# Kernel tuning notes

Measured on AMD Instinct MI355X. Metric: run time of the kernel, lower is better.

## Reference

```python
import jax, jax.numpy as jnp
import numpy as np

HEAD = 16
DIM = 1024
HEAD_DIM = DIM // HEAD


def setup_inputs() -> dict:
    key = jax.random.key(0)
    k1, k2, k3, k4 = jax.random.split(key, 4)
    x = jax.random.normal(k1, (2, 2048, DIM), dtype=jnp.float32)
    # nn.Linear(dim, 3*dim, bias=False): weight [3*dim, dim]
    w_qkv = jax.random.normal(k2, (3 * DIM, DIM), dtype=jnp.float32) * (DIM ** -0.5)
    # output proj nn.Linear(dim, dim)
    w_out = jax.random.normal(k3, (DIM, DIM), dtype=jnp.float32) * (DIM ** -0.5)
    b_out = jax.random.normal(k4, (DIM,), dtype=jnp.float32) * 0.01
    return {"x": x, "w_qkv": w_qkv, "w_out": w_out, "b_out": b_out}


def reference(x, w_qkv, w_out, b_out):
    b, s, _ = x.shape
    scale = HEAD_DIM ** -0.5
    qkv = jnp.einsum('bsd,ed->bse', x, w_qkv)  # [b, s, 3*dim]
    q, k, v = jnp.split(qkv, 3, axis=-1)
    def split_heads(t):
        return t.reshape(b, s, HEAD, HEAD_DIM).transpose(0, 2, 1, 3)  # b h s d
    q, k, v = split_heads(q), split_heads(k), split_heads(v)
    scores = jnp.einsum('bhqd,bhkd->bhqk', q, k) * scale
    attn = jax.nn.softmax(scores, axis=-1)
    out = jnp.einsum('bhqk,bhkd->bhqd', attn, v)
    out = out.transpose(0, 2, 1, 3).reshape(b, s, DIM)
    out = jnp.einsum('bsd,ed->bse', out, w_out) + b_out
    return out
```

## Files before the change

kernel.cpp:

```cpp
#include <hip/hip_runtime.h>
#include <hip/hip_bf16.h>
#include <stdint.h>

typedef __bf16 bf16_t;
typedef __attribute__((ext_vector_type(8))) __bf16 bf16x8;
typedef __attribute__((ext_vector_type(4))) __bf16 bf16x4v;
typedef __attribute__((ext_vector_type(4))) float f32x4;

#define GLOBAL_AS __attribute__((address_space(1)))
#define LDS_AS __attribute__((address_space(3)))

__device__ __forceinline__ void gload_lds16(const bf16_t* g, bf16_t* l) {
  __builtin_amdgcn_global_load_lds((const GLOBAL_AS void*)g, (LDS_AS void*)l, 16, 0, 0);
}

__device__ __forceinline__ uint32_t pk2(float a, float b) {
  union { bf16_t h[2]; uint32_t u; } x;
  x.h[0] = (bf16_t)a; x.h[1] = (bf16_t)b;
  return x.u;
}

__device__ __forceinline__ bf16x8 xpose8(bf16x8 v, int l) {
  union { bf16x8 v; uint32_t u[4]; } tv; tv.v = v;
  uint32_t a0 = __shfl_xor((int)tv.u[2], 4, 64);
  uint32_t a1 = __shfl_xor((int)tv.u[3], 4, 64);
  uint32_t a2 = __shfl_xor((int)tv.u[0], 4, 64);
  uint32_t a3 = __shfl_xor((int)tv.u[1], 4, 64);
  bool s4 = (l & 4) != 0;
  uint32_t n0 = s4 ? a0 : tv.u[0];
  uint32_t n1 = s4 ? a1 : tv.u[1];
  uint32_t n2 = s4 ? tv.u[2] : a2;
  uint32_t n3 = s4 ? tv.u[3] : a3;
  uint32_t b0 = __shfl_xor((int)n1, 2, 64);
  uint32_t b1 = __shfl_xor((int)n0, 2, 64);
  uint32_t b2 = __shfl_xor((int)n3, 2, 64);
  uint32_t b3 = __shfl_xor((int)n2, 2, 64);
  bool s2 = (l & 2) != 0;
  uint32_t m0 = s2 ? b0 : n0;
  uint32_t m1 = s2 ? n1 : b1;
  uint32_t m2 = s2 ? b2 : n2;
  uint32_t m3 = s2 ? n3 : b3;
  uint32_t c0 = __shfl_xor((int)m0, 1, 64);
  uint32_t c1 = __shfl_xor((int)m1, 1, 64);
  uint32_t c2 = __shfl_xor((int)m2, 1, 64);
  uint32_t c3 = __shfl_xor((int)m3, 1, 64);
  bool odd = (l & 1) != 0;
  union { uint32_t u[4]; bf16x8 v; } tw;
  tw.u[0] = odd ? ((m0 & 0xFFFF0000u) | (c0 >> 16)) : ((m0 & 0xFFFFu) | (c0 << 16));
  tw.u[1] = odd ? ((m1 & 0xFFFF0000u) | (c1 >> 16)) : ((m1 & 0xFFFFu) | (c1 << 16));
  tw.u[2] = odd ? ((m2 & 0xFFFF0000u) | (c2 >> 16)) : ((m2 & 0xFFFFu) | (c2 << 16));
  tw.u[3] = odd ? ((m3 & 0xFFFF0000u) | (c3 >> 16)) : ((m3 & 0xFFFFu) | (c3 << 16));
  return tw.v;
}

__global__ void cvt_f32_bf16(const float* __restrict__ in, bf16_t* __restrict__ out, int n) {
  int i = (blockIdx.x * 256 + threadIdx.x) * 4;
  if (i + 3 < n) {
    float4 v = *(const float4*)(in + i);
    bf16x4v o;
    o[0] = (bf16_t)v.x; o[1] = (bf16_t)v.y; o[2] = (bf16_t)v.z; o[3] = (bf16_t)v.w;
    *(bf16x4v*)(out + i) = o;
  }
}

template<int EPI>
__global__ __launch_bounds__(256)
void gemm_tn(const bf16_t* __restrict__ A, const bf16_t* __restrict__ B,
             void* __restrict__ Cout, const float* __restrict__ bias,
             int K, int ldc, int qcols, float qscale)
{
  __shared__ __align__(16) bf16_t As[128 * 32];
  __shared__ __align__(16) bf16_t Bs[128 * 32];
  const int t  = threadIdx.x;
  const int l  = t & 63, w = t >> 6;
  const int wm = w >> 1, wn = w & 1;
  const int lo = l & 15, hi = l >> 4;
  const int brow = blockIdx.y * 128;
  const int bcol = blockIdx.x * 128;

  const int i0 = t, i1 = t + 256;
  const int r0 = i0 >> 2, c0 = i0 & 3;
  const int r1 = i1 >> 2, c1 = i1 & 3;

  f32x4 acc[4][4] = {};

  for (int k0 = 0; k0 < K; k0 += 32) {
    gload_lds16(A + (size_t)(brow + r0) * K + k0 + c0 * 8, As + i0 * 8);
    gload_lds16(A + (size_t)(brow + r1) * K + k0 + c1 * 8, As + i1 * 8);
    gload_lds16(B + (size_t)(bcol + r0) * K + k0 + c0 * 8, Bs + i0 * 8);
    gload_lds16(B + (size_t)(bcol + r1) * K + k0 + c1 * 8, Bs + i1 * 8);
    __syncthreads();

    bf16x8 a[4], bb[4];
#pragma unroll
    for (int fm = 0; fm < 4; fm++)
      a[fm] = *(const bf16x8*)(As + (wm * 64 + fm * 16 + lo) * 32 + hi * 8);
#pragma unroll
    for (int fn = 0; fn < 4; fn++)
      bb[fn] = *(const bf16x8*)(Bs + (wn * 64 + fn * 16 + lo) * 32 + hi * 8);

#pragma unroll
    for (int fm = 0; fm < 4; fm++)
#pragma unroll
      for (int fn = 0; fn < 4; fn++)
        acc[fm][fn] = __builtin_amdgcn_mfma_f32_16x16x32_bf16(a[fm], bb[fn], acc[fm][fn], 0, 0, 0);
    __syncthreads();
  }

#pragma unroll
  for (int fm = 0; fm < 4; fm++) {
#pragma unroll
    for (int fn = 0; fn < 4; fn++) {
#pragma unroll
      for (int j = 0; j < 4; j++) {
        int row = brow + wm * 64 + fm * 16 + hi * 4 + j;
        int col = bcol + wn * 64 + fn * 16 + lo;
        float v = acc[fm][fn][j];
        if (EPI == 0) {
          if (col < qcols) v *= qscale;
          ((bf16_t*)Cout)[(size_t)row * ldc + col] = (bf16_t)v;
        } else {
          ((float*)Cout)[(size_t)row * ldc + col] = v + bias[col];
        }
      }
    }
  }
}

#define LDK 72

__global__ __launch_bounds__(512, 4)
void flash_attn(const bf16_t* __restrict__ qkv, bf16_t* __restrict__ aout)
{
  __shared__ __align__(16) bf16_t Kl[2][64 * LDK];
  __shared__ __align__(16) bf16_t Vt[2][64 * LDK];

  const int t = threadIdx.x;
  const int l = t & 63, w = t >> 6;
  const int lo = l & 15, hi = l >> 4;
  int bid = (int)blockIdx.x;
  bid = (bid & 7) * 64 + (bid >> 3);
  const int qblk = bid & 15;
  const int bh   = bid >> 4;
  const int b = bh >> 4, h = bh & 15;
  const int rowbase = b * 2048;
  const int q0 = qblk * 128 + w * 16;

  const int r = l & 7, c = l >> 3;
  const int krow = w * 8 + (l >> 3);
  const int kc   = l & 7;
  const int vkey = 32 * (w >> 2) + 16 * (r >> 2) + 4 * (w & 3) + (r & 3);
  const bf16_t* kvbase = qkv + (size_t)rowbase * 3072 + h * 64 + 1024;
  const size_t step = (size_t)64 * 3072;

  bf16x8 aq[2];
#pragma unroll
  for (int kb = 0; kb < 2; kb++)
    aq[kb] = *(const bf16x8*)(qkv + (size_t)(rowbase + q0 + lo) * 3072
                              + h * 64 + kb * 32 + hi * 8);

  bf16x8 ones;
#pragma unroll
  for (int j = 0; j < 8; j++) ones[j] = (bf16_t)1.0f;

  f32x4 oacc[4] = {};
  f32x4 ssum = {};

  bf16x8 kch = *(const bf16x8*)(kvbase + (size_t)krow * 3072 + kc * 8);
  bf16x8 vch = *(const bf16x8*)(kvbase + 1024 + (size_t)vkey * 3072 + c * 8);
  *(bf16x8*)(&Kl[0][0] + krow * LDK + kc * 8) = kch;
  *(bf16x8*)(&Vt[0][0] + (c * 8 + r) * LDK + w * 8) = xpose8(vch, l);

  const bf16_t* kv_next = kvbase + step;
  kch = *(const bf16x8*)(kv_next + (size_t)krow * 3072 + kc * 8);
  vch = *(const bf16x8*)(kv_next + 1024 + (size_t)vkey * 3072 + c * 8);
  kv_next += step;

  for (int it = 0; it < 32; ++it) {
    __syncthreads();
    const int cur = it & 1;
    bf16_t* KlN = &Kl[cur ^ 1][0];
    bf16_t* VtN = &Vt[cur ^ 1][0];
    const bf16_t* KlC = &Kl[cur][0];
    const bf16_t* VtC = &Vt[cur][0];

    if (it < 31) {
      *(bf16x8*)(KlN + krow * LDK + kc * 8) = kch;
      *(bf16x8*)(VtN + (c * 8 + r) * LDK + w * 8) = xpose8(vch, l);
    }
    if (it < 30) {
      kch = *(const bf16x8*)(kv_next + (size_t)krow * 3072 + kc * 8);
      vch = *(const bf16x8*)(kv_next + 1024 + (size_t)vkey * 3072 + c * 8);
      kv_next += step;
    }

    bf16x8 kf[4][2];
#pragma unroll
    for (int fn = 0; fn < 4; fn++)
#pragma unroll
      for (int kb = 0; kb < 2; kb++)
        kf[fn][kb] = *(const bf16x8*)(KlC + (fn * 16 + lo) * LDK + kb * 32 + hi * 8);
    f32x4 sacc[4] = {};
    __builtin_amdgcn_s_setprio(1);
#pragma unroll
    for (int fn = 0; fn < 4; fn++)
#pragma unroll
      for (int kb = 0; kb < 2; kb++)
        sacc[fn] = __builtin_amdgcn_mfma_f32_16x16x32_bf16(kf[fn][kb], aq[kb], sacc[fn], 0, 0, 0);
    __builtin_amdgcn_s_setprio(0);

    float p[4][4];
#pragma unroll
    for (int fn = 0; fn < 4; fn++)
#pragma unroll
      for (int j = 0; j < 4; j++)
        p[fn][j] = __builtin_amdgcn_exp2f(sacc[fn][j]);
    bf16x8 pa[2];
#pragma unroll
    for (int kb = 0; kb < 2; kb++) {
      union { uint32_t u[4]; bf16x8 v; } pw;
      pw.u[0] = pk2(p[2 * kb][0],     p[2 * kb][1]);
      pw.u[1] = pk2(p[2 * kb][2],     p[2 * kb][3]);
      pw.u[2] = pk2(p[2 * kb + 1][0], p[2 * kb + 1][1]);
      pw.u[3] = pk2(p[2 * kb + 1][2], p[2 * kb + 1][3]);
      pa[kb] = pw.v;
    }

    bf16x8 vb[4][2];
#pragma unroll
    for (int fd = 0; fd < 4; fd++)
#pragma unroll
      for (int kb = 0; kb < 2; kb++)
        vb[fd][kb] = *(const bf16x8*)(VtC + (fd * 16 + lo) * LDK + kb * 32 + hi * 8);
    __builtin_amdgcn_s_setprio(1);
#pragma unroll
    for (int kb = 0; kb < 2; kb++)
      ssum = __builtin_amdgcn_mfma_f32_16x16x32_bf16(pa[kb], ones, ssum, 0, 0, 0);
#pragma unroll
    for (int fd = 0; fd < 4; fd++)
#pragma unroll
      for (int kb = 0; kb < 2; kb++)
        oacc[fd] = __builtin_amdgcn_mfma_f32_16x16x32_bf16(pa[kb], vb[fd][kb], oacc[fd], 0, 0, 0);
    __builtin_amdgcn_s_setprio(0);
  }

#pragma unroll
  for (int j = 0; j < 4; j++) {
    float inv = 1.0f / ssum[j];
    int row = rowbase + q0 + hi * 4 + j;
#pragma unroll
    for (int fd = 0; fd < 4; fd++) {
      int col = h * 64 + fd * 16 + lo;
      aout[(size_t)row * 1024 + col] = (bf16_t)(oacc[fd][j] * inv);
    }
  }
}

extern "C" void kernel_launch(void* const* d_in, const int* in_sizes, int n_in,
                              void* d_out, int out_size, void* d_ws, size_t ws_size,
                              hipStream_t stream) {
  const float* x     = (const float*)d_in[0];
  const float* w_qkv = (const float*)d_in[1];
  const float* w_out = (const float*)d_in[2];
  const float* b_out = (const float*)d_in[3];

  char* ws = (char*)d_ws;
  bf16_t* xb   = (bf16_t*)(ws);
  bf16_t* wqb  = (bf16_t*)(ws + 8388608);
  bf16_t* wob  = (bf16_t*)(ws + 14680064);
  bf16_t* qkvb = (bf16_t*)(ws + 16777216);
  bf16_t* aob  = (bf16_t*)(ws + 41943040);

  cvt_f32_bf16<<<4096, 256, 0, stream>>>(x,     xb,  4194304);
  cvt_f32_bf16<<<3072, 256, 0, stream>>>(w_qkv, wqb, 3145728);
  cvt_f32_bf16<<<1024, 256, 0, stream>>>(w_out, wob, 1048576);

  dim3 g1(24, 32);
  gemm_tn<0><<<g1, 256, 0, stream>>>(xb, wqb, qkvb, nullptr, 1024, 3072, 1024, 0.18033688011f);

  flash_attn<<<512, 512, 0, stream>>>(qkvb, aob);

  dim3 g2(8, 32);
  gemm_tn<1><<<g2, 256, 0, stream>>>(aob, wob, d_out, b_out, 1024, 1024, 0, 1.0f);
}
```

Measured before the change: 141.1 us.

## Halve flash-attention block size to 4 waves and double grid size

Flash attention now runs 256-thread blocks covering 64 query rows each, launched as 1024 blocks instead of 512 blocks of 128 rows. Each thread loads and stages two K and two V chunks per tile, with the staging index mapping and block swizzle reworked to match. This is meant to give more blocks for scheduling across CUs and better load balance. The cost is that each K/V tile is loaded from global memory by twice as many blocks, doubling K/V traffic.

```diff
diff --git a/kernel.cpp b/kernel.cpp
--- a/kernel.cpp
+++ b/kernel.cpp
@@ -129,7 +129,7 @@
 
 #define LDK 72
 
-__global__ __launch_bounds__(512, 4)
+__global__ __launch_bounds__(256, 4)
 void flash_attn(const bf16_t* __restrict__ qkv, bf16_t* __restrict__ aout)
 {
   __shared__ __align__(16) bf16_t Kl[2][64 * LDK];
@@ -139,17 +139,16 @@
   const int l = t & 63, w = t >> 6;
   const int lo = l & 15, hi = l >> 4;
   int bid = (int)blockIdx.x;
-  bid = (bid & 7) * 64 + (bid >> 3);
-  const int qblk = bid & 15;
-  const int bh   = bid >> 4;
+  bid = (bid & 7) * 128 + (bid >> 3);
+  const int qblk = bid & 31;
+  const int bh   = bid >> 5;
   const int b = bh >> 4, h = bh & 15;
   const int rowbase = b * 2048;
-  const int q0 = qblk * 128 + w * 16;
+  const int q0 = qblk * 64 + w * 16;
 
   const int r = l & 7, c = l >> 3;
-  const int krow = w * 8 + (l >> 3);
-  const int kc   = l & 7;
-  const int vkey = 32 * (w >> 2) + 16 * (r >> 2) + 4 * (w & 3) + (r & 3);
+  const int krow_w = w * 16 + r;
+  const int vkey_w = 32 * (w >> 1) + 8 * (w & 1) + 16 * (r >> 2) + (r & 3);
   const bf16_t* kvbase = qkv + (size_t)rowbase * 3072 + h * 64 + 1024;
   const size_t step = (size_t)64 * 3072;
 
@@ -166,14 +165,23 @@
   f32x4 oacc[4] = {};
   f32x4 ssum = {};
 
-  bf16x8 kch = *(const bf16x8*)(kvbase + (size_t)krow * 3072 + kc * 8);
-  bf16x8 vch = *(const bf16x8*)(kvbase + 1024 + (size_t)vkey * 3072 + c * 8);
-  *(bf16x8*)(&Kl[0][0] + krow * LDK + kc * 8) = kch;
-  *(bf16x8*)(&Vt[0][0] + (c * 8 + r) * LDK + w * 8) = xpose8(vch, l);
-
+  bf16x8 kch[2], vch[2];
+#pragma unroll
+  for (int i = 0; i < 2; i++) {
+    kch[i] = *(const bf16x8*)(kvbase + (size_t)(krow_w + 8 * i) * 3072 + c * 8);
+    vch[i] = *(const bf16x8*)(kvbase + 1024 + (size_t)(vkey_w + 4 * i) * 3072 + c * 8);
+  }
+#pragma unroll
+  for (int i = 0; i < 2; i++) {
+    *(bf16x8*)(&Kl[0][0] + (krow_w + 8 * i) * LDK + c * 8) = kch[i];
+    *(bf16x8*)(&Vt[0][0] + (c * 8 + r) * LDK + w * 16 + i * 8) = xpose8(vch[i], l);
+  }
   const bf16_t* kv_next = kvbase + step;
-  kch = *(const bf16x8*)(kv_next + (size_t)krow * 3072 + kc * 8);
-  vch = *(const bf16x8*)(kv_next + 1024 + (size_t)vkey * 3072 + c * 8);
+#pragma unroll
+  for (int i = 0; i < 2; i++) {
+    kch[i] = *(const bf16x8*)(kv_next + (size_t)(krow_w + 8 * i) * 3072 + c * 8);
+    vch[i] = *(const bf16x8*)(kv_next + 1024 + (size_t)(vkey_w + 4 * i) * 3072 + c * 8);
+  }
   kv_next += step;
 
   for (int it = 0; it < 32; ++it) {
@@ -185,12 +193,18 @@
     const bf16_t* VtC = &Vt[cur][0];
 
     if (it < 31) {
-      *(bf16x8*)(KlN + krow * LDK + kc * 8) = kch;
-      *(bf16x8*)(VtN + (c * 8 + r) * LDK + w * 8) = xpose8(vch, l);
+#pragma unroll
+      for (int i = 0; i < 2; i++) {
+        *(bf16x8*)(KlN + (krow_w + 8 * i) * LDK + c * 8) = kch[i];
+        *(bf16x8*)(VtN + (c * 8 + r) * LDK + w * 16 + i * 8) = xpose8(vch[i], l);
+      }
     }
     if (it < 30) {
-      kch = *(const bf16x8*)(kv_next + (size_t)krow * 3072 + kc * 8);
-      vch = *(const bf16x8*)(kv_next + 1024 + (size_t)vkey * 3072 + c * 8);
+#pragma unroll
+      for (int i = 0; i < 2; i++) {
+        kch[i] = *(const bf16x8*)(kv_next + (size_t)(krow_w + 8 * i) * 3072 + c * 8);
+        vch[i] = *(const bf16x8*)(kv_next + 1024 + (size_t)(vkey_w + 4 * i) * 3072 + c * 8);
+      }
       kv_next += step;
     }
 
@@ -278,7 +292,7 @@
   dim3 g1(24, 32);
   gemm_tn<0><<<g1, 256, 0, stream>>>(xb, wqb, qkvb, nullptr, 1024, 3072, 1024, 0.18033688011f);
 
-  flash_attn<<<512, 512, 0, stream>>>(qkvb, aob);
+  flash_attn<<<1024, 256, 0, stream>>>(qkvb, aob);
 
   dim3 g2(8, 32);
   gemm_tn<1><<<g2, 256, 0, stream>>>(aob, wob, d_out, b_out, 1024, 1024, 0, 1.0f);
```

After: 164.0 us. +16.3%, slower.

## Split flash attention over KV halves with atomic fp32 accumulation and normalize pass

Applied to the files above, without the earlier changes.

Splits each (batch, head, query-block) attention job into two blocks, each covering half of the key/value sequence. This doubles the grid to 1024 blocks for more parallelism on the CUs. Each block atomically adds its unnormalized output and row sums into fp32 buffers, which are zeroed beforehand by memsets. A new elementwise kernel then divides by the sums and writes bf16. This adds memset, atomic and extra pass traffic, and the tighter launch bound (512,8) may force register spills.

```diff
diff --git a/kernel.cpp b/kernel.cpp
--- a/kernel.cpp
+++ b/kernel.cpp
@@ -129,8 +129,9 @@
 
 #define LDK 72
 
-__global__ __launch_bounds__(512, 4)
-void flash_attn(const bf16_t* __restrict__ qkv, bf16_t* __restrict__ aout)
+__global__ __launch_bounds__(512, 8)
+void flash_part(const bf16_t* __restrict__ qkv, float* __restrict__ Oacc,
+                float* __restrict__ Ssum)
 {
   __shared__ __align__(16) bf16_t Kl[2][64 * LDK];
   __shared__ __align__(16) bf16_t Vt[2][64 * LDK];
@@ -138,10 +139,11 @@
   const int t = threadIdx.x;
   const int l = t & 63, w = t >> 6;
   const int lo = l & 15, hi = l >> 4;
-  int bid = (int)blockIdx.x;
-  bid = (bid & 7) * 64 + (bid >> 3);
-  const int qblk = bid & 15;
-  const int bh   = bid >> 4;
+  const int x = (int)blockIdx.x;
+  const int cxcd = x & 7, m = x >> 3;
+  const int qblk = m & 15, gh = m >> 4;
+  const int g = gh * 8 + cxcd;
+  const int bh = g >> 1, half = g & 1;
   const int b = bh >> 4, h = bh & 15;
   const int rowbase = b * 2048;
   const int q0 = qblk * 128 + w * 16;
@@ -150,8 +152,9 @@
   const int krow = w * 8 + (l >> 3);
   const int kc   = l & 7;
   const int vkey = 32 * (w >> 2) + 16 * (r >> 2) + 4 * (w & 3) + (r & 3);
-  const bf16_t* kvbase = qkv + (size_t)rowbase * 3072 + h * 64 + 1024;
   const size_t step = (size_t)64 * 3072;
+  const bf16_t* kvbase = qkv + (size_t)rowbase * 3072 + h * 64 + 1024
+                       + (size_t)(half * 16) * step;
 
   bf16x8 aq[2];
 #pragma unroll
@@ -176,7 +179,7 @@
   vch = *(const bf16x8*)(kv_next + 1024 + (size_t)vkey * 3072 + c * 8);
   kv_next += step;
 
-  for (int it = 0; it < 32; ++it) {
+  for (int it = 0; it < 16; ++it) {
     __syncthreads();
     const int cur = it & 1;
     bf16_t* KlN = &Kl[cur ^ 1][0];
@@ -184,11 +187,11 @@
     const bf16_t* KlC = &Kl[cur][0];
     const bf16_t* VtC = &Vt[cur][0];
 
-    if (it < 31) {
+    if (it < 15) {
       *(bf16x8*)(KlN + krow * LDK + kc * 8) = kch;
       *(bf16x8*)(VtN + (c * 8 + r) * LDK + w * 8) = xpose8(vch, l);
     }
-    if (it < 30) {
+    if (it < 14) {
       kch = *(const bf16x8*)(kv_next + (size_t)krow * 3072 + kc * 8);
       vch = *(const bf16x8*)(kv_next + 1024 + (size_t)vkey * 3072 + c * 8);
       kv_next += step;
@@ -246,14 +249,29 @@
 
 #pragma unroll
   for (int j = 0; j < 4; j++) {
-    float inv = 1.0f / ssum[j];
     int row = rowbase + q0 + hi * 4 + j;
+    if (lo == 0) atomicAdd(&Ssum[row * 16 + h], ssum[j]);
 #pragma unroll
     for (int fd = 0; fd < 4; fd++) {
       int col = h * 64 + fd * 16 + lo;
-      aout[(size_t)row * 1024 + col] = (bf16_t)(oacc[fd][j] * inv);
-    }
-  }
+      atomicAdd(&Oacc[(size_t)row * 1024 + col], oacc[fd][j]);
+    }
+  }
+}
+
+__global__ void norm_attn(const float* __restrict__ Oacc, const float* __restrict__ Ssum,
+                          bf16_t* __restrict__ aob)
+{
+  int i = blockIdx.x * 256 + threadIdx.x;
+  int base = i * 4;
+  float4 o = *(const float4*)(Oacc + base);
+  int row = base >> 10;
+  int col = base & 1023;
+  float inv = 1.0f / Ssum[row * 16 + (col >> 6)];
+  bf16x4v rr;
+  rr[0] = (bf16_t)(o.x * inv); rr[1] = (bf16_t)(o.y * inv);
+  rr[2] = (bf16_t)(o.z * inv); rr[3] = (bf16_t)(o.w * inv);
+  *(bf16x4v*)(aob + base) = rr;
 }
 
 extern "C" void kernel_launch(void* const* d_in, const int* in_sizes, int n_in,
@@ -270,6 +288,8 @@
   bf16_t* wob  = (bf16_t*)(ws + 14680064);
   bf16_t* qkvb = (bf16_t*)(ws + 16777216);
   bf16_t* aob  = (bf16_t*)(ws + 41943040);
+  float*  ssum = (float*)(ws);
+  float*  oaccf = (float*)d_out;
 
   cvt_f32_bf16<<<4096, 256, 0, stream>>>(x,     xb,  4194304);
   cvt_f32_bf16<<<3072, 256, 0, stream>>>(w_qkv, wqb, 3145728);
@@ -278,7 +298,11 @@
   dim3 g1(24, 32);
   gemm_tn<0><<<g1, 256, 0, stream>>>(xb, wqb, qkvb, nullptr, 1024, 3072, 1024, 0.18033688011f);
 
-  flash_attn<<<512, 512, 0, stream>>>(qkvb, aob);
+  hipMemsetAsync(oaccf, 0, (size_t)4096 * 1024 * 4, stream);
+  hipMemsetAsync(ssum, 0, (size_t)4096 * 16 * 4, stream);
+
+  flash_part<<<1024, 512, 0, stream>>>(qkvb, oaccf, ssum);
+  norm_attn<<<4096, 256, 0, stream>>>(oaccf, ssum, aob);
 
   dim3 g2(8, 32);
   gemm_tn<1><<<g2, 256, 0, stream>>>(aob, wob, d_out, b_out, 1024, 1024, 0, 1.0f);
```

Result: slower. 276.5 us (+96.0%).
